# Kernel tuning notes

Hardware: AMD Instinct MI355X
Metric: run time of the kernel (lower is better)

Reference implementation:

```python
import jax, jax.numpy as jnp
import numpy as np
import math

EPS = 1e-6          # eps for safe cumprod / clamping
CHUNK = 4           # chunk_size w
SHARP = 1.0         # sharpening_factor
NOISE_STD = 1.0
N_HEADS = 4
ADIM = 512


def moving_sum(x, back, forward):
    """Windowed running sum over last axis: out[k] = sum_{j=k-back}^{k+forward} x[j].
    Equivalent to the conv1d trick in the original (all-ones filter)."""
    k = x.shape[-1]
    pad = [(0, 0)] * (x.ndim - 1) + [(back, forward)]
    c = jnp.cumsum(jnp.pad(x, pad), axis=-1)
    c0 = jnp.concatenate([jnp.zeros_like(c[..., :1]), c], axis=-1)
    w = back + forward
    return c0[..., w + 1: w + 1 + k] - c0[..., :k]


def setup_inputs() -> dict:
    rng = jax.random.key(0)
    ks = jax.random.split(rng, 12)
    B, qlen, klen, kdim, qdim, adim = 8, 256, 2048, 512, 512, ADIM
    s = 0.02
    return {
        "key_enc": jax.random.normal(ks[0], (B, klen, kdim), jnp.float32),
        "query":   jax.random.normal(ks[1], (B, qlen, qdim), jnp.float32),
        "noise":   jax.random.normal(ks[2], (B, qlen, klen), jnp.float32),
        # monotonic energy params
        "Wk_m": jax.random.normal(ks[3], (kdim, adim), jnp.float32) * s,
        "bk_m": jnp.zeros((adim,), jnp.float32),
        "Wq_m": jax.random.normal(ks[4], (qdim, adim), jnp.float32) * s,
        "bq_m": jnp.zeros((adim,), jnp.float32),
        "r":    jnp.array([-4.0], jnp.float32),
        # chunkwise energy params (multi-head)
        "Wk_c": jax.random.normal(ks[5], (kdim, adim), jnp.float32) * s,
        "bk_c": jnp.zeros((adim,), jnp.float32),
        "Wq_c": jax.random.normal(ks[6], (qdim, adim), jnp.float32) * s,
        "bq_c": jnp.zeros((adim,), jnp.float32),
    }


def _mocha_beta(key_enc, query, noise, Wk_m, bk_m, Wq_m, bq_m, r,
                Wk_c, bk_c, Wq_c, bq_c):
    B, klen, _ = key_enc.shape
    qlen = query.shape[1]
    H = N_HEADS
    dk = ADIM // H
    scale = math.sqrt(ADIM)

    # --- monotonic energy (single head): [B, qlen, klen]
    k_m = key_enc @ Wk_m + bk_m
    q_m = query @ Wq_m + bq_m
    e_mono = jnp.einsum('bqa,bka->bqk', q_m, k_m) / scale + r[0]

    # --- p_choose with additive gaussian noise (encourages discreteness)
    p_choose = jax.nn.sigmoid(e_mono + noise * NOISE_STD)  # [B,q,k]

    # --- safe cumprod of (1 - p) via exclusive cumsum in log space
    log1mp = jnp.log(jnp.clip(1.0 - p_choose, EPS, 1.0))
    cumprod_1mp = jnp.exp(jnp.cumsum(log1mp, axis=-1) - log1mp)  # exclusive

    # --- monotonic alpha recurrence over query steps (parallel-mode MoChA)
    aw0 = jnp.zeros((B, klen), jnp.float32).at[:, 0].set(1.0)

    def step(aw_prev, inp):
        p_i, cp_i = inp  # [B, klen]
        alpha_i = p_i * cp_i * jnp.cumsum(
            aw_prev / jnp.clip(cp_i, EPS, 1.0), axis=-1)
        return alpha_i, alpha_i

    xs = (jnp.swapaxes(p_choose, 0, 1), jnp.swapaxes(cumprod_1mp, 0, 1))
    _, alpha_q = jax.lax.scan(step, aw0, xs)          # [q, B, k]
    alpha = jnp.swapaxes(alpha_q, 0, 1)                # [B, q, k]

    # --- chunkwise energy (multi-head): [B, H, q, k]
    k_c = (key_enc @ Wk_c + bk_c).reshape(B, klen, H, dk)
    q_c = (query @ Wq_c + bq_c).reshape(B, qlen, H, dk)
    e_chunk = jnp.einsum('bqhd,bkhd->bhqk', q_c, k_c) / scale

    # --- efficient chunkwise attention (clipped-logit moving-sum softmax)
    e = e_chunk - jnp.max(e_chunk, axis=3, keepdims=True)
    softmax_exp = jnp.maximum(jnp.exp(e), 1e-5)
    denom = moving_sum(softmax_exp, back=CHUNK - 1, forward=0)
    beta = softmax_exp * moving_sum(
        alpha[:, None] * SHARP / denom, back=0, forward=CHUNK - 1)
    return beta  # [B, H, q, k]


def reference(key_enc, query, noise, Wk_m, bk_m, Wq_m, bq_m, r,
              Wk_c, bk_c, Wq_c, bq_c):
    return _mocha_beta(key_enc, query, noise, Wk_m, bk_m, Wq_m, bq_m, r,
                       Wk_c, bk_c, Wq_c, bq_c)
```

## Files before the change

### kernel.cpp

```cpp
#include <hip/hip_runtime.h>
#include <math.h>

#define BATCH   8
#define QLEN    256
#define KLEN    2048
#define KDIM    512
#define ADIMC   512
#define NHEADS  4
#define DKH     128
#define CHUNKW  4

static constexpr float INV_SCALE = 0.04419417382415922f;
static constexpr float EPSV = 1e-6f;

typedef __attribute__((ext_vector_type(8))) short bf16x8;
typedef __attribute__((ext_vector_type(4))) float f32x4;

__device__ __forceinline__ unsigned short f2bf(float f) {
    unsigned u = __builtin_bit_cast(unsigned, f);
    u += 0x7fffu + ((u >> 16) & 1u);
    return (unsigned short)(u >> 16);
}

__device__ __forceinline__ void lds_barrier() {
    __asm__ volatile("s_waitcnt lgkmcnt(0)\n\ts_barrier" ::: "memory");
}

__device__ __forceinline__ void gload_lds16(const void* g, void* l) {
    __builtin_amdgcn_global_load_lds(
        (const __attribute__((address_space(1))) void*)g,
        (__attribute__((address_space(3))) void*)l, 16, 0, 0);
}

__global__ __launch_bounds__(256) void cast_bf16(
    const float* __restrict__ x, unsigned short* __restrict__ y, int n4)
{
    int i = blockIdx.x * 256 + threadIdx.x;
    if (i < n4) {
        float4 v = ((const float4*)x)[i];
        ushort4 o;
        o.x = f2bf(v.x); o.y = f2bf(v.y); o.z = f2bf(v.z); o.w = f2bf(v.w);
        ((ushort4*)y)[i] = o;
    }
}

__global__ __launch_bounds__(256) void transpose_cast(
    const float* __restrict__ W, unsigned short* __restrict__ WT)
{
    __shared__ float tile[32][33];
    const int tx = threadIdx.x;
    const int ty = threadIdx.y;
    const int k0 = blockIdx.y * 32, n0 = blockIdx.x * 32;
    #pragma unroll
    for (int i = 0; i < 32; i += 8)
        tile[ty + i][tx] = W[(size_t)(k0 + ty + i) * KDIM + n0 + tx];
    __syncthreads();
    #pragma unroll
    for (int i = 0; i < 32; i += 8)
        WT[(size_t)(n0 + ty + i) * KDIM + k0 + tx] = f2bf(tile[tx][ty + i]);
}

template<int KSTEPS>
__device__ __forceinline__ void mfma_nt_staged(
    const unsigned short* __restrict__ A, const unsigned short* __restrict__ B,
    int lda, int ldb, int bm, int bn,
    unsigned short* AsLDS, unsigned short* BsLDS, f32x4 acc[4][4])
{
    const int t = threadIdx.x;
    const int wv = t >> 6, ln = t & 63;
    const int r = ln & 15, quad = ln >> 4;
    const int wm = (wv >> 1) * 64, wn = (wv & 1) * 64;
    const int srow = wv * 16 + (ln >> 2);
    const int scol = (ln & 3) * 8;

    for (int ks = 0; ks < KSTEPS; ++ks) {
        const int k0 = ks * 32;
        #pragma unroll
        for (int j = 0; j < 2; ++j) {
            gload_lds16(A + (size_t)(bm + j * 64 + srow) * lda + k0 + scol,
                        AsLDS + (size_t)(j * 64 + wv * 16) * 32);
            gload_lds16(B + (size_t)(bn + j * 64 + srow) * ldb + k0 + scol,
                        BsLDS + (size_t)(j * 64 + wv * 16) * 32);
        }
        __syncthreads();
        bf16x8 af[4], bg[4];
        #pragma unroll
        for (int f = 0; f < 4; ++f)
            af[f] = *(const bf16x8*)(AsLDS + (size_t)(wm + f * 16 + r) * 32 + quad * 8);
        #pragma unroll
        for (int f = 0; f < 4; ++f)
            bg[f] = *(const bf16x8*)(BsLDS + (size_t)(wn + f * 16 + r) * 32 + quad * 8);
        #pragma unroll
        for (int i = 0; i < 4; ++i)
            #pragma unroll
            for (int j2 = 0; j2 < 4; ++j2)
                acc[i][j2] = __builtin_amdgcn_mfma_f32_16x16x32_bf16(
                    af[i], bg[j2], acc[i][j2], 0, 0, 0);
        __syncthreads();
    }
}

__device__ __forceinline__ void zero_acc(f32x4 acc[4][4]) {
    #pragma unroll
    for (int i = 0; i < 4; ++i)
        #pragma unroll
        for (int j = 0; j < 4; ++j)
            acc[i][j] = f32x4{0.f, 0.f, 0.f, 0.f};
}

__global__ __launch_bounds__(256) void proj_mfma(
    const unsigned short* __restrict__ A, const unsigned short* __restrict__ WT,
    const float* __restrict__ bias_m, const float* __restrict__ bias_c,
    unsigned short* __restrict__ C)
{
    __shared__ unsigned short As[128 * 32];
    __shared__ unsigned short Bs[128 * 32];
    const int bm = blockIdx.y * 128, bn = blockIdx.x * 128;
    f32x4 acc[4][4]; zero_acc(acc);
    mfma_nt_staged<16>(A, WT, KDIM, KDIM, bm, bn, As, Bs, acc);
    const int wv = threadIdx.x >> 6, ln = threadIdx.x & 63;
    const int r = ln & 15, quad = ln >> 4;
    const int m0 = bm + (wv >> 1) * 64, n0 = bn + (wv & 1) * 64;
    #pragma unroll
    for (int j = 0; j < 4; ++j) {
        const int n = n0 + j * 16 + r;
        const float bv = (n < 512) ? bias_m[n] : bias_c[n - 512];
        #pragma unroll
        for (int i = 0; i < 4; ++i) {
            #pragma unroll
            for (int reg = 0; reg < 4; ++reg) {
                const int m = m0 + i * 16 + quad * 4 + reg;
                C[(size_t)m * 1024 + n] = f2bf(acc[i][j][reg] + bv);
            }
        }
    }
}

__global__ __launch_bounds__(256) void pchoose_mfma(
    const unsigned short* __restrict__ qp, const unsigned short* __restrict__ kp,
    const float* __restrict__ noise, const float* __restrict__ rp,
    float* __restrict__ p)
{
    __shared__ unsigned short As[128 * 32];
    __shared__ unsigned short Bs[128 * 32];
    const int b = blockIdx.z;
    const unsigned short* A = qp + (size_t)b * QLEN * 1024;
    const unsigned short* B = kp + (size_t)b * KLEN * 1024;
    const int bm = blockIdx.y * 128, bn = blockIdx.x * 128;
    f32x4 acc[4][4]; zero_acc(acc);
    mfma_nt_staged<16>(A, B, 1024, 1024, bm, bn, As, Bs, acc);
    const int wv = threadIdx.x >> 6, ln = threadIdx.x & 63;
    const int r = ln & 15, quad = ln >> 4;
    const int m0 = bm + (wv >> 1) * 64, n0 = bn + (wv & 1) * 64;
    const float rv = rp[0];
    #pragma unroll
    for (int i = 0; i < 4; ++i) {
        #pragma unroll
        for (int reg = 0; reg < 4; ++reg) {
            const int q = m0 + i * 16 + quad * 4 + reg;
            const size_t rowoff = ((size_t)b * QLEN + q) * KLEN;
            #pragma unroll
            for (int j = 0; j < 4; ++j) {
                const int k = n0 + j * 16 + r;
                const float e = acc[i][j][reg] * INV_SCALE + rv + noise[rowoff + k];
                p[rowoff + k] = __builtin_amdgcn_rcpf(1.0f + __expf(-e));
            }
        }
    }
}

__device__ __forceinline__ float wave_incl_scan(float x)
{
#define DPP_ADD(ctrl, rmask, bctrl)                                            \
    { int _t = __builtin_amdgcn_update_dpp(0, __builtin_bit_cast(int, x),      \
                                           ctrl, rmask, 0xf, bctrl);           \
      x += __builtin_bit_cast(float, _t); }
    DPP_ADD(0x111, 0xf, true)
    DPP_ADD(0x112, 0xf, true)
    DPP_ADD(0x114, 0xf, true)
    DPP_ADD(0x118, 0xf, true)
    DPP_ADD(0x142, 0xa, false)
    DPP_ADD(0x143, 0xc, false)
#undef DPP_ADD
    return x;
}

__global__ __launch_bounds__(256) void cumprod_mr(
    const float* __restrict__ p, float* __restrict__ mArr, float* __restrict__ rArr)
{
    const size_t row = blockIdx.x;
    const float* pr = p + row * KLEN;
    float* mr = mArr + row * KLEN;
    float* rr = rArr + row * KLEN;
    const int tid = threadIdx.x;
    const int lane = tid & 63, wid = tid >> 6;
    __shared__ float waveTot[4];

    float4 v0 = *(const float4*)(pr + tid * 8);
    float4 v1 = *(const float4*)(pr + tid * 8 + 4);
    float pv[8] = {v0.x, v0.y, v0.z, v0.w, v1.x, v1.y, v1.z, v1.w};
    float excl[8];
    float run = 0.0f;
    #pragma unroll
    for (int j = 0; j < 8; ++j) {
        float l = __logf(fminf(fmaxf(1.0f - pv[j], EPSV), 1.0f));
        excl[j] = run;
        run += l;
    }
    float s = wave_incl_scan(run);
    if (lane == 63) waveTot[wid] = s;
    __syncthreads();
    float wex = 0.0f;
    for (int w = 0; w < wid; ++w) wex += waveTot[w];
    const float texcl = wex + s - run;

    float mv[8], rv[8];
    #pragma unroll
    for (int j = 0; j < 8; ++j) {
        const float cpv = __expf(texcl + excl[j]);
        mv[j] = pv[j] * cpv;
        rv[j] = __builtin_amdgcn_rcpf(fminf(fmaxf(cpv, EPSV), 1.0f));
    }
    *(float4*)(mr + tid * 8)     = *(float4*)&mv[0];
    *(float4*)(mr + tid * 8 + 4) = *(float4*)&mv[4];
    *(float4*)(rr + tid * 8)     = *(float4*)&rv[0];
    *(float4*)(rr + tid * 8 + 4) = *(float4*)&rv[4];
}

__global__ __launch_bounds__(512, 1) void alpha_echunk(
    const float* __restrict__ mArr, const float* __restrict__ rArr,
    float* __restrict__ alpha,
    const unsigned short* __restrict__ qp, const unsigned short* __restrict__ kp,
    float* __restrict__ out)
{
    __shared__ __align__(16) char smem[98304];
    const int bid = blockIdx.x;
    const int tid = threadIdx.x;

    if (bid < BATCH) {
        __builtin_amdgcn_s_setprio(1);
        float (*wt)[8] = (float (*)[8])smem;
        const int lane = tid & 63, wid = tid >> 6;
        const float* mrow = mArr + (size_t)bid * QLEN * KLEN + tid * 4;
        const float* rrow = rArr + (size_t)bid * QLEN * KLEN + tid * 4;
        float* arow = alpha + (size_t)bid * QLEN * KLEN + tid * 4;

        float aw0 = 0.f, aw1 = 0.f, aw2 = 0.f, aw3 = 0.f;
        if (tid == 0) aw0 = 1.0f;

        float4 mA = *(const float4*)(mrow);
        float4 rA = *(const float4*)(rrow);
        float4 mB = *(const float4*)(mrow + KLEN);
        float4 rB = *(const float4*)(rrow + KLEN);

#define ASTEP(I, MREG, RREG)                                                   \
    {                                                                          \
        const int i_ = (I);                                                    \
        float4 mc = MREG, rc = RREG;                                           \
        const int rn_ = (i_ + 2 < QLEN) ? (i_ + 2) : (QLEN - 1);               \
        MREG = *(const float4*)(mrow + (size_t)rn_ * KLEN);                    \
        RREG = *(const float4*)(rrow + (size_t)rn_ * KLEN);                    \
        float run = 0.0f, i0, i1, i2, i3;                                      \
        run = fmaf(aw0, rc.x, run); i0 = run;                                  \
        run = fmaf(aw1, rc.y, run); i1 = run;                                  \
        run = fmaf(aw2, rc.z, run); i2 = run;                                  \
        run = fmaf(aw3, rc.w, run); i3 = run;                                  \
        float tot = wave_incl_scan(run);                                       \
        if (lane == 63) wt[i_ & 1][wid] = tot;                                 \
        lds_barrier();                                                         \
        float base = tot - run;                                                \
        float4 w0 = *(const float4*)&wt[i_ & 1][0];                            \
        float4 w1 = *(const float4*)&wt[i_ & 1][4];                            \
        if (wid > 0) base += w0.x;                                             \
        if (wid > 1) base += w0.y;                                             \
        if (wid > 2) base += w0.z;                                             \
        if (wid > 3) base += w0.w;                                             \
        if (wid > 4) base += w1.x;                                             \
        if (wid > 5) base += w1.y;                                             \
        if (wid > 6) base += w1.z;                                             \
        aw0 = mc.x * (base + i0);                                              \
        aw1 = mc.y * (base + i1);                                              \
        aw2 = mc.z * (base + i2);                                              \
        aw3 = mc.w * (base + i3);                                              \
        float4 ov; ov.x = aw0; ov.y = aw1; ov.z = aw2; ov.w = aw3;             \
        *(float4*)(arow + (size_t)i_ * KLEN) = ov;                             \
    }

        for (int io = 0; io < QLEN; io += 2) {
            ASTEP(io + 0, mA, rA)
            ASTEP(io + 1, mB, rB)
        }
#undef ASTEP
        __builtin_amdgcn_s_setprio(0);
        return;
    }

    const int v = bid - BATCH;
    const int z = v >> 5;
    const int by = (v >> 4) & 1;
    const int bx = v & 15;
    const int b = z >> 2, h = z & 3;
    const bool worker = tid < 256;
    unsigned short* As = (unsigned short*)smem;
    unsigned short* Bs = (unsigned short*)(smem + 8192);
    const unsigned short* A = qp + (size_t)b * QLEN * 1024 + 512 + h * DKH;
    const unsigned short* B = kp + (size_t)b * KLEN * 1024 + 512 + h * DKH;
    const int bm = by * 128, bn = bx * 128;

    const int wv = tid >> 6, ln = tid & 63;
    const int r = ln & 15, quad = ln >> 4;
    const int wm = (wv >> 1) * 64, wn = (wv & 1) * 64;
    const int srow = (wv & 3) * 16 + (ln >> 2);
    const int scol = (ln & 3) * 8;

    f32x4 acc[4][4]; zero_acc(acc);
    for (int ks = 0; ks < 4; ++ks) {
        const int k0 = ks * 32;
        if (worker) {
            #pragma unroll
            for (int j = 0; j < 2; ++j) {
                gload_lds16(A + (size_t)(bm + j * 64 + srow) * 1024 + k0 + scol,
                            As + (size_t)(j * 64 + wv * 16) * 32);
                gload_lds16(B + (size_t)(bn + j * 64 + srow) * 1024 + k0 + scol,
                            Bs + (size_t)(j * 64 + wv * 16) * 32);
            }
        }
        __syncthreads();
        if (worker) {
            bf16x8 af[4], bg[4];
            #pragma unroll
            for (int f = 0; f < 4; ++f)
                af[f] = *(const bf16x8*)(As + (size_t)(wm + f * 16 + r) * 32 + quad * 8);
            #pragma unroll
            for (int f = 0; f < 4; ++f)
                bg[f] = *(const bf16x8*)(Bs + (size_t)(wn + f * 16 + r) * 32 + quad * 8);
            #pragma unroll
            for (int i = 0; i < 4; ++i)
                #pragma unroll
                for (int j2 = 0; j2 < 4; ++j2)
                    acc[i][j2] = __builtin_amdgcn_mfma_f32_16x16x32_bf16(
                        af[i], bg[j2], acc[i][j2], 0, 0, 0);
        }
        __syncthreads();
    }
    if (worker) {
        const int m0 = bm + (wv >> 1) * 64, n0 = bn + (wv & 1) * 64;
        #pragma unroll
        for (int i = 0; i < 4; ++i) {
            #pragma unroll
            for (int reg = 0; reg < 4; ++reg) {
                const int q = m0 + i * 16 + quad * 4 + reg;
                const size_t rowoff = ((size_t)z * QLEN + q) * KLEN;
                #pragma unroll
                for (int j = 0; j < 4; ++j) {
                    const int k = n0 + j * 16 + r;
                    out[rowoff + k] = acc[i][j][reg] * INV_SCALE;
                }
            }
        }
    }
}

__global__ __launch_bounds__(256) void beta_kernel(
    float* __restrict__ eo, const float* __restrict__ alpha)
{
    __shared__ float sse[KLEN + 3];
    __shared__ float su[KLEN + 3];
    __shared__ float wmax[4];

    const int tid = threadIdx.x;
    const int lane = tid & 63, wid = tid >> 6;
    const int row = blockIdx.x;
    const int q = row & (QLEN - 1);
    const int b = row >> 10;
    float* erow = eo + (size_t)row * KLEN;
    const float* arow = alpha + ((size_t)b * QLEN + q) * KLEN;

    if (tid < 3) { sse[tid] = 0.0f; su[KLEN + tid] = 0.0f; }

// ... 21 lines not shown
    #pragma unroll
    for (int j = 0; j < 8; ++j) {
        const int k = tid + 256 * j;
        const float denom = sse[k + 3] + sse[k + 2] + sse[k + 1] + sse[k];
        su[k] = arow[k] * __builtin_amdgcn_rcpf(denom);
    }
    __syncthreads();

    #pragma unroll
    for (int j = 0; j < 8; ++j) {
        const int k = tid + 256 * j;
        erow[k] = sse[k + 3] * (su[k] + su[k + 1] + su[k + 2] + su[k + 3]);
    }
}

extern "C" void kernel_launch(void* const* d_in, const int* in_sizes, int n_in,
                              void* d_out, int out_size, void* d_ws, size_t ws_size,
                              hipStream_t stream)
{
    (void)in_sizes; (void)n_in; (void)out_size; (void)ws_size;
    const float* key_enc = (const float*)d_in[0];
    const float* query   = (const float*)d_in[1];
    const float* noise   = (const float*)d_in[2];
    const float* Wk_m    = (const float*)d_in[3];
    const float* bk_m    = (const float*)d_in[4];
    const float* Wq_m    = (const float*)d_in[5];
    const float* bq_m    = (const float*)d_in[6];
    const float* rp      = (const float*)d_in[7];
    const float* Wk_c    = (const float*)d_in[8];
    const float* bk_c    = (const float*)d_in[9];
    const float* Wq_c    = (const float*)d_in[10];
    const float* bq_c    = (const float*)d_in[11];
    float* out = (float*)d_out;

    char* w = (char*)d_ws;
    unsigned short* kx    = (unsigned short*)w; w += (size_t)BATCH * KLEN * KDIM * 2;
    unsigned short* qx    = (unsigned short*)w; w += (size_t)BATCH * QLEN * KDIM * 2;
    unsigned short* WTk   = (unsigned short*)w; w += (size_t)1024 * KDIM * 2;
    unsigned short* WTq   = (unsigned short*)w; w += (size_t)1024 * KDIM * 2;
    unsigned short* kproj = (unsigned short*)w; w += (size_t)BATCH * KLEN * 1024 * 2;
    unsigned short* qproj = (unsigned short*)w; w += (size_t)BATCH * QLEN * 1024 * 2;
    float* p_alpha = (float*)w; w += (size_t)BATCH * QLEN * KLEN * 4;
    float* mArr    = (float*)w; w += (size_t)BATCH * QLEN * KLEN * 4;
    float* rArr    = (float*)w;

    hipLaunchKernelGGL(cast_bf16, dim3(BATCH * KLEN * KDIM / 4 / 256), dim3(256), 0, stream,
                       key_enc, kx, BATCH * KLEN * KDIM / 4);
    hipLaunchKernelGGL(cast_bf16, dim3(BATCH * QLEN * KDIM / 4 / 256), dim3(256), 0, stream,
                       query, qx, BATCH * QLEN * KDIM / 4);
    hipLaunchKernelGGL(transpose_cast, dim3(16, 16), dim3(32, 8), 0, stream, Wk_m, WTk);
    hipLaunchKernelGGL(transpose_cast, dim3(16, 16), dim3(32, 8), 0, stream, Wk_c, WTk + (size_t)512 * KDIM);
    hipLaunchKernelGGL(transpose_cast, dim3(16, 16), dim3(32, 8), 0, stream, Wq_m, WTq);
    hipLaunchKernelGGL(transpose_cast, dim3(16, 16), dim3(32, 8), 0, stream, Wq_c, WTq + (size_t)512 * KDIM);

    hipLaunchKernelGGL(proj_mfma, dim3(8, BATCH * KLEN / 128), dim3(256), 0, stream,
                       kx, WTk, bk_m, bk_c, kproj);
    hipLaunchKernelGGL(proj_mfma, dim3(8, BATCH * QLEN / 128), dim3(256), 0, stream,
                       qx, WTq, bq_m, bq_c, qproj);

    hipLaunchKernelGGL(pchoose_mfma, dim3(KLEN / 128, QLEN / 128, BATCH), dim3(256), 0, stream,
                       qproj, kproj, noise, rp, p_alpha);

    hipLaunchKernelGGL(cumprod_mr, dim3(BATCH * QLEN), dim3(256), 0, stream,
                       p_alpha, mArr, rArr);

    hipLaunchKernelGGL(alpha_echunk, dim3(BATCH + KLEN / 128 * QLEN / 128 * BATCH * NHEADS),
                       dim3(512), 0, stream,
                       mArr, rArr, p_alpha, qproj, kproj, out);

    hipLaunchKernelGGL(beta_kernel, dim3(BATCH * NHEADS * QLEN), dim3(256), 0, stream,
                       out, p_alpha);
}
```

Before: 307.6 us.

## Replace per-step block barrier in alpha scan with LDS flag-chained wave prefix passing

The sequential alpha recurrence used a block-wide s_barrier each query step to combine the eight waves' partial sums. It now uses a decoupled chained scan: each wave spins on a 64-bit LDS slot holding the previous wave's inclusive prefix tagged with the step index, then publishes its own. This removes the full-block barrier from the critical path but makes the waves a serial chain and adds volatile LDS polling. It also costs one up-front zeroing pass over QLEN*8 slots.

```diff
diff --git a/kernel.cpp b/kernel.cpp
--- a/kernel.cpp
+++ b/kernel.cpp
@@ -20,10 +20,6 @@
     unsigned u = __builtin_bit_cast(unsigned, f);
     u += 0x7fffu + ((u >> 16) & 1u);
     return (unsigned short)(u >> 16);
-}
-
-__device__ __forceinline__ void lds_barrier() {
-    __asm__ volatile("s_waitcnt lgkmcnt(0)\n\ts_barrier" ::: "memory");
 }
 
 __device__ __forceinline__ void gload_lds16(const void* g, void* l) {
@@ -238,13 +234,19 @@
     const int tid = threadIdx.x;
 
     if (bid < BATCH) {
+        unsigned long long* slots = (unsigned long long*)smem;
+        for (int idx = tid; idx < QLEN * 8; idx += 512) slots[idx] = 0ULL;
+        __syncthreads();
+
         __builtin_amdgcn_s_setprio(1);
-        float (*wt)[8] = (float (*)[8])smem;
         const int lane = tid & 63, wid = tid >> 6;
         const float* mrow = mArr + (size_t)bid * QLEN * KLEN + tid * 4;
         const float* rrow = rArr + (size_t)bid * QLEN * KLEN + tid * 4;
         float* arow = alpha + (size_t)bid * QLEN * KLEN + tid * 4;
 
+        volatile unsigned long long* psl  = slots + ((wid > 0) ? (wid - 1) : 0);
+        volatile unsigned long long* pslw = slots + wid;
+
         float aw0 = 0.f, aw1 = 0.f, aw2 = 0.f, aw3 = 0.f;
         if (tid == 0) aw0 = 1.0f;
 
@@ -256,6 +258,8 @@
 #define ASTEP(I, MREG, RREG)                                                   \
     {                                                                          \
         const int i_ = (I);                                                    \
+        unsigned long long v_ = 0ULL;                                          \
+        if (wid > 0) v_ = *psl;             \
         float4 mc = MREG, rc = RREG;                                           \
         const int rn_ = (i_ + 2 < QLEN) ? (i_ + 2) : (QLEN - 1);               \
         MREG = *(const float4*)(mrow + (size_t)rn_ * KLEN);                    \
@@ -265,23 +269,21 @@
         run = fmaf(aw1, rc.y, run); i1 = run;                                  \
         run = fmaf(aw2, rc.z, run); i2 = run;                                  \
         run = fmaf(aw3, rc.w, run); i3 = run;                                  \
-        float tot = wave_incl_scan(run);                                       \
-        if (lane == 63) wt[i_ & 1][wid] = tot;                                 \
-        lds_barrier();                                                         \
-        float base = tot - run;                                                \
-        float4 w0 = *(const float4*)&wt[i_ & 1][0];                            \
-        float4 w1 = *(const float4*)&wt[i_ & 1][4];                            \
-        if (wid > 0) base += w0.x;                                             \
-        if (wid > 1) base += w0.y;                                             \
-        if (wid > 2) base += w0.z;                                             \
-        if (wid > 3) base += w0.w;                                             \
-        if (wid > 4) base += w1.x;                                             \
-        if (wid > 5) base += w1.y;                                             \
-        if (wid > 6) base += w1.z;                                             \
-        aw0 = mc.x * (base + i0);                                              \
-        aw1 = mc.y * (base + i1);                                              \
-        aw2 = mc.z * (base + i2);                                              \
-        aw3 = mc.w * (base + i3);                                              \
+        float s_ = wave_incl_scan(run);                                        \
+        float base = 0.0f;                                                     \
+        if (wid > 0) {                                                         \
+            while ((unsigned)(v_ >> 32) != (unsigned)(i_ + 1)) v_ = *psl;      \
+            base = __builtin_bit_cast(float, (unsigned)v_);                    \
+        }                                                                      \
+        if (wid < 7 && lane == 63)                                             \
+            *pslw = ((unsigned long long)(unsigned)(i_ + 1) << 32)             \
+                  | (unsigned long long)__builtin_bit_cast(unsigned, base + s_);\
+        psl += 8; pslw += 8;                                                   \
+        const float wb = base + (s_ - run);                                    \
+        aw0 = mc.x * (wb + i0);                                                \
+        aw1 = mc.y * (wb + i1);                                                \
+        aw2 = mc.z * (wb + i2);                                                \
+        aw3 = mc.w * (wb + i3);                                                \
         float4 ov; ov.x = aw0; ov.y = aw1; ov.z = aw2; ov.w = aw3;             \
         *(float4*)(arow + (size_t)i_ * KLEN) = ov;                             \
     }
```

After: 402.2 us. 30.8% more time.

## Merge prep and projection launches; shrink alpha_echunk blocks to 256 threads

Applied to the files above, without the earlier changes.

The two cast kernels and four transpose-cast kernels become one prep launch, and the two projection GEMMs become one launch split by block row, cutting launch count and letting small grids share the device. The alpha_echunk kernel goes from 512 to 256 threads: the serial alpha scan now handles 8 columns per thread over 4 waves, which shortens the cross-wave reduction. The e_chunk GEMM blocks lose their idle half of threads. The risk is a longer per-thread serial chain in the scan, which sits on the critical path.

```diff
diff --git a/kernel.cpp b/kernel.cpp
--- a/kernel.cpp
+++ b/kernel.cpp
@@ -32,25 +32,40 @@
         (__attribute__((address_space(3))) void*)l, 16, 0, 0);
 }
 
-__global__ __launch_bounds__(256) void cast_bf16(
-    const float* __restrict__ x, unsigned short* __restrict__ y, int n4)
-{
-    int i = blockIdx.x * 256 + threadIdx.x;
-    if (i < n4) {
+#define NKXB (BATCH * KLEN * KDIM / 4 / 256)
+#define NQXB (BATCH * QLEN * KDIM / 4 / 256)
+__global__ __launch_bounds__(256) void prep(
+    const float* __restrict__ key_enc, const float* __restrict__ query,
+    const float* __restrict__ Wk_m, const float* __restrict__ Wk_c,
+    const float* __restrict__ Wq_m, const float* __restrict__ Wq_c,
+    unsigned short* __restrict__ kx, unsigned short* __restrict__ qx,
+    unsigned short* __restrict__ WTk, unsigned short* __restrict__ WTq)
+{
+    __shared__ float tile[32][33];
+    const int gb = blockIdx.x;
+    const int tid = threadIdx.x;
+
+    if (gb < NKXB + NQXB) {
+        const float* x = (gb < NKXB) ? key_enc : query;
+        unsigned short* y = (gb < NKXB) ? kx : qx;
+        const int i = (gb < NKXB ? gb : gb - NKXB) * 256 + tid;
         float4 v = ((const float4*)x)[i];
         ushort4 o;
         o.x = f2bf(v.x); o.y = f2bf(v.y); o.z = f2bf(v.z); o.w = f2bf(v.w);
         ((ushort4*)y)[i] = o;
-    }
-}
-
-__global__ __launch_bounds__(256) void transpose_cast(
-    const float* __restrict__ W, unsigned short* __restrict__ WT)
-{
-    __shared__ float tile[32][33];
-    const int tx = threadIdx.x;
-    const int ty = threadIdx.y;
-    const int k0 = blockIdx.y * 32, n0 = blockIdx.x * 32;
+        return;
+    }
+    const int t = gb - NKXB - NQXB;
+    const int which = t >> 8;
+    const int tt = t & 255;
+    const int bx = tt & 15, byy = tt >> 4;
+    const float* W = (which == 0) ? Wk_m : (which == 1) ? Wk_c
+                   : (which == 2) ? Wq_m : Wq_c;
+    unsigned short* WT = (which == 0) ? WTk
+                       : (which == 1) ? WTk + (size_t)512 * KDIM
+                       : (which == 2) ? WTq : WTq + (size_t)512 * KDIM;
+    const int tx = tid & 31, ty = tid >> 5;
+    const int k0 = byy * 32, n0 = bx * 32;
     #pragma unroll
     for (int i = 0; i < 32; i += 8)
         tile[ty + i][tx] = W[(size_t)(k0 + ty + i) * KDIM + n0 + tx];
@@ -109,13 +124,22 @@
 }
 
 __global__ __launch_bounds__(256) void proj_mfma(
-    const unsigned short* __restrict__ A, const unsigned short* __restrict__ WT,
-    const float* __restrict__ bias_m, const float* __restrict__ bias_c,
-    unsigned short* __restrict__ C)
+    const unsigned short* __restrict__ kx, const unsigned short* __restrict__ qx,
+    const unsigned short* __restrict__ WTk, const unsigned short* __restrict__ WTq,
+    const float* __restrict__ bk_m, const float* __restrict__ bk_c,
+    const float* __restrict__ bq_m, const float* __restrict__ bq_c,
+    unsigned short* __restrict__ kproj, unsigned short* __restrict__ qproj)
 {
     __shared__ unsigned short As[128 * 32];
     __shared__ unsigned short Bs[128 * 32];
-    const int bm = blockIdx.y * 128, bn = blockIdx.x * 128;
+    const int by = blockIdx.y;
+    const unsigned short *A, *WT;
+    unsigned short* C;
+    const float *bm_, *bc_;
+    int bm;
+    if (by < 128) { A = kx; WT = WTk; C = kproj; bm_ = bk_m; bc_ = bk_c; bm = by * 128; }
+    else          { A = qx; WT = WTq; C = qproj; bm_ = bq_m; bc_ = bq_c; bm = (by - 128) * 128; }
+    const int bn = blockIdx.x * 128;
     f32x4 acc[4][4]; zero_acc(acc);
     mfma_nt_staged<16>(A, WT, KDIM, KDIM, bm, bn, As, Bs, acc);
     const int wv = threadIdx.x >> 6, ln = threadIdx.x & 63;
@@ -124,7 +148,7 @@
     #pragma unroll
     for (int j = 0; j < 4; ++j) {
         const int n = n0 + j * 16 + r;
-        const float bv = (n < 512) ? bias_m[n] : bias_c[n - 512];
+        const float bv = (n < 512) ? bm_[n] : bc_[n - 512];
         #pragma unroll
         for (int i = 0; i < 4; ++i) {
             #pragma unroll
@@ -227,7 +251,7 @@
     *(float4*)(rr + tid * 8 + 4) = *(float4*)&rv[4];
 }
 
-__global__ __launch_bounds__(512, 1) void alpha_echunk(
+__global__ __launch_bounds__(256, 1) void alpha_echunk(
     const float* __restrict__ mArr, const float* __restrict__ rArr,
     float* __restrict__ alpha,
     const unsigned short* __restrict__ qp, const unsigned short* __restrict__ kp,
@@ -239,56 +263,68 @@
 
     if (bid < BATCH) {
         __builtin_amdgcn_s_setprio(1);
-        float (*wt)[8] = (float (*)[8])smem;
+        float (*wt)[4] = (float (*)[4])smem;
         const int lane = tid & 63, wid = tid >> 6;
-        const float* mrow = mArr + (size_t)bid * QLEN * KLEN + tid * 4;
-        const float* rrow = rArr + (size_t)bid * QLEN * KLEN + tid * 4;
-        float* arow = alpha + (size_t)bid * QLEN * KLEN + tid * 4;
+        const float* mrow = mArr + (size_t)bid * QLEN * KLEN + tid * 8;
+        const float* rrow = rArr + (size_t)bid * QLEN * KLEN + tid * 8;
+        float* arow = alpha + (size_t)bid * QLEN * KLEN + tid * 8;
 
         float aw0 = 0.f, aw1 = 0.f, aw2 = 0.f, aw3 = 0.f;
+        float aw4 = 0.f, aw5 = 0.f, aw6 = 0.f, aw7 = 0.f;
         if (tid == 0) aw0 = 1.0f;
 
-        float4 mA = *(const float4*)(mrow);
-        float4 rA = *(const float4*)(rrow);
-        float4 mB = *(const float4*)(mrow + KLEN);
-        float4 rB = *(const float4*)(rrow + KLEN);
-
-#define ASTEP(I, MREG, RREG)                                                   \
+        float4 mA0 = *(const float4*)(mrow);
+        float4 mA1 = *(const float4*)(mrow + 4);
+        float4 rA0 = *(const float4*)(rrow);
+        float4 rA1 = *(const float4*)(rrow + 4);
+        float4 mB0 = *(const float4*)(mrow + KLEN);
+        float4 mB1 = *(const float4*)(mrow + KLEN + 4);
+        float4 rB0 = *(const float4*)(rrow + KLEN);
+        float4 rB1 = *(const float4*)(rrow + KLEN + 4);
+
+#define ASTEP(I, M0, M1, R0, R1)                                               \
     {                                                                          \
         const int i_ = (I);                                                    \
-        float4 mc = MREG, rc = RREG;                                           \
+        float4 mc0 = M0, mc1 = M1, rc0 = R0, rc1 = R1;                         \
         const int rn_ = (i_ + 2 < QLEN) ? (i_ + 2) : (QLEN - 1);               \
-        MREG = *(const float4*)(mrow + (size_t)rn_ * KLEN);                    \
-        RREG = *(const float4*)(rrow + (size_t)rn_ * KLEN);                    \
-        float run = 0.0f, i0, i1, i2, i3;                                      \
-        run = fmaf(aw0, rc.x, run); i0 = run;                                  \
-        run = fmaf(aw1, rc.y, run); i1 = run;                                  \
-        run = fmaf(aw2, rc.z, run); i2 = run;                                  \
-        run = fmaf(aw3, rc.w, run); i3 = run;                                  \
+        M0 = *(const float4*)(mrow + (size_t)rn_ * KLEN);                      \
+        M1 = *(const float4*)(mrow + (size_t)rn_ * KLEN + 4);                  \
+        R0 = *(const float4*)(rrow + (size_t)rn_ * KLEN);                      \
+        R1 = *(const float4*)(rrow + (size_t)rn_ * KLEN + 4);                  \
+        float run = 0.0f, i0, i1, i2, i3, i4, i5, i6, i7;                      \
+        run = fmaf(aw0, rc0.x, run); i0 = run;                                 \
+        run = fmaf(aw1, rc0.y, run); i1 = run;                                 \
+        run = fmaf(aw2, rc0.z, run); i2 = run;                                 \
+        run = fmaf(aw3, rc0.w, run); i3 = run;                                 \
+        run = fmaf(aw4, rc1.x, run); i4 = run;                                 \
+        run = fmaf(aw5, rc1.y, run); i5 = run;                                 \
+        run = fmaf(aw6, rc1.z, run); i6 = run;                                 \
+        run = fmaf(aw7, rc1.w, run); i7 = run;                                 \
         float tot = wave_incl_scan(run);                                       \
         if (lane == 63) wt[i_ & 1][wid] = tot;                                 \
         lds_barrier();                                                         \
         float base = tot - run;                                                \
         float4 w0 = *(const float4*)&wt[i_ & 1][0];                            \
-        float4 w1 = *(const float4*)&wt[i_ & 1][4];                            \
         if (wid > 0) base += w0.x;                                             \
         if (wid > 1) base += w0.y;                                             \
         if (wid > 2) base += w0.z;                                             \
-        if (wid > 3) base += w0.w;                                             \
-        if (wid > 4) base += w1.x;                                             \
-        if (wid > 5) base += w1.y;                                             \
-        if (wid > 6) base += w1.z;                                             \
-        aw0 = mc.x * (base + i0);                                              \
-        aw1 = mc.y * (base + i1);                                              \
-        aw2 = mc.z * (base + i2);                                              \
-        aw3 = mc.w * (base + i3);                                              \
-        float4 ov; ov.x = aw0; ov.y = aw1; ov.z = aw2; ov.w = aw3;             \
-        *(float4*)(arow + (size_t)i_ * KLEN) = ov;                             \
+        aw0 = mc0.x * (base + i0);                                             \
+        aw1 = mc0.y * (base + i1);                                             \
+        aw2 = mc0.z * (base + i2);                                             \
+        aw3 = mc0.w * (base + i3);                                             \
+        aw4 = mc1.x * (base + i4);                                             \
+        aw5 = mc1.y * (base + i5);                                             \
+        aw6 = mc1.z * (base + i6);                                             \
+        aw7 = mc1.w * (base + i7);                                             \
+        float4 ov0; ov0.x = aw0; ov0.y = aw1; ov0.z = aw2; ov0.w = aw3;        \
+        float4 ov1; ov1.x = aw4; ov1.y = aw5; ov1.z = aw6; ov1.w = aw7;        \
+        *(float4*)(arow + (size_t)i_ * KLEN)     = ov0;                        \
+        *(float4*)(arow + (size_t)i_ * KLEN + 4) = ov1;                        \
     }
 
         for (int io = 0; io < QLEN; io += 2) {
-            ASTEP(io + 0, mA, rA)
-            ASTEP(io + 1, mB, rB)
+            ASTEP(io + 0, mA0, mA1, rA0, rA1)
+            ASTEP(io + 1, mB0, mB1, rB0, rB1)
         }
 #undef ASTEP
         __builtin_amdgcn_s_setprio(0);
@@ -300,7 +336,6 @@
     const int by = (v >> 4) & 1;
     const int bx = v & 15;
     const int b = z >> 2, h = z & 3;
-    const bool worker = tid < 256;
     unsigned short* As = (unsigned short*)smem;
     unsigned short* Bs = (unsigned short*)(smem + 8192);
     const unsigned short* A = qp + (size_t)b * QLEN * 1024 + 512 + h * DKH;
@@ -310,40 +345,36 @@
     const int wv = tid >> 6, ln = tid & 63;
     const int r = ln & 15, quad = ln >> 4;
     const int wm = (wv >> 1) * 64, wn = (wv & 1) * 64;
-    const int srow = (wv & 3) * 16 + (ln >> 2);
+    const int srow = wv * 16 + (ln >> 2);
     const int scol = (ln & 3) * 8;
 
     f32x4 acc[4][4]; zero_acc(acc);
     for (int ks = 0; ks < 4; ++ks) {
         const int k0 = ks * 32;
-        if (worker) {
+        #pragma unroll
+        for (int j = 0; j < 2; ++j) {
+            gload_lds16(A + (size_t)(bm + j * 64 + srow) * 1024 + k0 + scol,
+                        As + (size_t)(j * 64 + wv * 16) * 32);
+            gload_lds16(B + (size_t)(bn + j * 64 + srow) * 1024 + k0 + scol,
+                        Bs + (size_t)(j * 64 + wv * 16) * 32);
+        }
+        __syncthreads();
+        bf16x8 af[4], bg[4];
+        #pragma unroll
+        for (int f = 0; f < 4; ++f)
+            af[f] = *(const bf16x8*)(As + (size_t)(wm + f * 16 + r) * 32 + quad * 8);
+        #pragma unroll
+        for (int f = 0; f < 4; ++f)
+            bg[f] = *(const bf16x8*)(Bs + (size_t)(wn + f * 16 + r) * 32 + quad * 8);
+        #pragma unroll
+        for (int i = 0; i < 4; ++i)
             #pragma unroll
-            for (int j = 0; j < 2; ++j) {
-                gload_lds16(A + (size_t)(bm + j * 64 + srow) * 1024 + k0 + scol,
-                            As + (size_t)(j * 64 + wv * 16) * 32);
-                gload_lds16(B + (size_t)(bn + j * 64 + srow) * 1024 + k0 + scol,
-                            Bs + (size_t)(j * 64 + wv * 16) * 32);
-            }
-        }
+            for (int j2 = 0; j2 < 4; ++j2)
+                acc[i][j2] = __builtin_amdgcn_mfma_f32_16x16x32_bf16(
+                    af[i], bg[j2], acc[i][j2], 0, 0, 0);
         __syncthreads();
-        if (worker) {
-            bf16x8 af[4], bg[4];
-            #pragma unroll
-            for (int f = 0; f < 4; ++f)
-                af[f] = *(const bf16x8*)(As + (size_t)(wm + f * 16 + r) * 32 + quad * 8);
-            #pragma unroll
-            for (int f = 0; f < 4; ++f)
-                bg[f] = *(const bf16x8*)(Bs + (size_t)(wn + f * 16 + r) * 32 + quad * 8);
-            #pragma unroll
-            for (int i = 0; i < 4; ++i)
-                #pragma unroll
-                for (int j2 = 0; j2 < 4; ++j2)
-                    acc[i][j2] = __builtin_amdgcn_mfma_f32_16x16x32_bf16(
-                        af[i], bg[j2], acc[i][j2], 0, 0, 0);
-        }
-        __syncthreads();
-    }
-    if (worker) {
+    }
+    {
         const int m0 = bm + (wv >> 1) * 64, n0 = bn + (wv & 1) * 64;
         #pragma unroll
         for (int i = 0; i < 4; ++i) {
@@ -444,19 +475,13 @@
     float* mArr    = (float*)w; w += (size_t)BATCH * QLEN * KLEN * 4;
     float* rArr    = (float*)w;
 
-    hipLaunchKernelGGL(cast_bf16, dim3(BATCH * KLEN * KDIM / 4 / 256), dim3(256), 0, stream,
-                       key_enc, kx, BATCH * KLEN * KDIM / 4);
-    hipLaunchKernelGGL(cast_bf16, dim3(BATCH * QLEN * KDIM / 4 / 256), dim3(256), 0, stream,
-                       query, qx, BATCH * QLEN * KDIM / 4);
-    hipLaunchKernelGGL(transpose_cast, dim3(16, 16), dim3(32, 8), 0, stream, Wk_m, WTk);
-    hipLaunchKernelGGL(transpose_cast, dim3(16, 16), dim3(32, 8), 0, stream, Wk_c, WTk + (size_t)512 * KDIM);
-    hipLaunchKernelGGL(transpose_cast, dim3(16, 16), dim3(32, 8), 0, stream, Wq_m, WTq);
-    hipLaunchKernelGGL(transpose_cast, dim3(16, 16), dim3(32, 8), 0, stream, Wq_c, WTq + (size_t)512 * KDIM);
-
-    hipLaunchKernelGGL(proj_mfma, dim3(8, BATCH * KLEN / 128), dim3(256), 0, stream,
-                       kx, WTk, bk_m, bk_c, kproj);
-    hipLaunchKernelGGL(proj_mfma, dim3(8, BATCH * QLEN / 128), dim3(256), 0, stream,
-                       qx, WTq, bq_m, bq_c, qproj);
+    hipLaunchKernelGGL(prep, dim3(NKXB + NQXB + 1024), dim3(256), 0, stream,
+                       key_enc, query, Wk_m, Wk_c, Wq_m, Wq_c,
+                       kx, qx, WTk, WTq);
+
+    hipLaunchKernelGGL(proj_mfma, dim3(8, BATCH * KLEN / 128 + BATCH * QLEN / 128),
+                       dim3(256), 0, stream,
+                       kx, qx, WTk, WTq, bk_m, bk_c, bq_m, bq_c, kproj, qproj);
 
     hipLaunchKernelGGL(pchoose_mfma, dim3(KLEN / 128, QLEN / 128, BATCH), dim3(256), 0, stream,
                        qproj, kproj, noise, rp, p_alpha);
@@ -465,7 +490,7 @@
                        p_alpha, mArr, rArr);
 
     hipLaunchKernelGGL(alpha_echunk, dim3(BATCH + KLEN / 128 * QLEN / 128 * BATCH * NHEADS),
-                       dim3(512), 0, stream,
+                       dim3(256), 0, stream,
                        mArr, rArr, p_alpha, qproj, kproj, out);
 
     hipLaunchKernelGGL(beta_kernel, dim3(BATCH * NHEADS * QLEN), dim3(256), 0, stream,
```

After: 296.6 us. 3.6% less time.

## Reassociate projections: fold key weights into query side, skip key projection GEMM

Applied to the files above, without the earlier changes.

Rather than projecting the large key tensor (B*2048 rows) through both weight matrices, precompute G = Wq·Wk^T per segment and per head, so that q·G can be multiplied directly against the raw bf16 keys. Bias cross-terms are folded into a per-column offset, and a per-query scalar replaces the bias terms in the monotonic energy. This removes the 16K-row key projection GEMM and its bf16 writeback, plus the weight transposes, in exchange for a wider query-side matrix (5×512 columns) and a K=512 inner loop in the chunk energy GEMM instead of 128. The cast kernels are merged into one launch, and the chunk-energy tiles become 128x256 using all 8 waves.

```diff
diff --git a/kernel.cpp b/kernel.cpp
--- a/kernel.cpp
+++ b/kernel.cpp
@@ -5,10 +5,11 @@
 #define QLEN    256
 #define KLEN    2048
 #define KDIM    512
-#define ADIMC   512
 #define NHEADS  4
 #define DKH     128
-#define CHUNKW  4
+#define NG      5
+#define QROWS   (BATCH * QLEN)
+#define GCOLS   (NG * 512)
 
 static constexpr float INV_SCALE = 0.04419417382415922f;
 static constexpr float EPSV = 1e-6f;
@@ -21,6 +22,10 @@
     u += 0x7fffu + ((u >> 16) & 1u);
     return (unsigned short)(u >> 16);
 }
+__device__ __forceinline__ float bf2f(unsigned short u) {
+    unsigned x = (unsigned)u << 16;
+    return __builtin_bit_cast(float, x);
+}
 
 __device__ __forceinline__ void lds_barrier() {
     __asm__ volatile("s_waitcnt lgkmcnt(0)\n\ts_barrier" ::: "memory");
@@ -32,39 +37,37 @@
         (__attribute__((address_space(3))) void*)l, 16, 0, 0);
 }
 
-__global__ __launch_bounds__(256) void cast_bf16(
-    const float* __restrict__ x, unsigned short* __restrict__ y, int n4)
-{
-    int i = blockIdx.x * 256 + threadIdx.x;
-    if (i < n4) {
-        float4 v = ((const float4*)x)[i];
-        ushort4 o;
-        o.x = f2bf(v.x); o.y = f2bf(v.y); o.z = f2bf(v.z); o.w = f2bf(v.w);
-        ((ushort4*)y)[i] = o;
-    }
-}
-
-__global__ __launch_bounds__(256) void transpose_cast(
-    const float* __restrict__ W, unsigned short* __restrict__ WT)
-{
-    __shared__ float tile[32][33];
-    const int tx = threadIdx.x;
-    const int ty = threadIdx.y;
-    const int k0 = blockIdx.y * 32, n0 = blockIdx.x * 32;
-    #pragma unroll
-    for (int i = 0; i < 32; i += 8)
-        tile[ty + i][tx] = W[(size_t)(k0 + ty + i) * KDIM + n0 + tx];
-    __syncthreads();
-    #pragma unroll
-    for (int i = 0; i < 32; i += 8)
-        WT[(size_t)(n0 + ty + i) * KDIM + k0 + tx] = f2bf(tile[tx][ty + i]);
-}
-
-template<int KSTEPS>
+#define NKXB 8192
+#define NQXB 1024
+__global__ __launch_bounds__(256) void prep(
+    const float* __restrict__ key_enc, const float* __restrict__ query,
+    const float* __restrict__ Wk_m, const float* __restrict__ Wk_c,
+    const float* __restrict__ Wq_m, const float* __restrict__ Wq_c,
+    unsigned short* __restrict__ kx, unsigned short* __restrict__ qx,
+    unsigned short* __restrict__ kwm, unsigned short* __restrict__ kwc,
+    unsigned short* __restrict__ qwm, unsigned short* __restrict__ qwc)
+{
+    const int gb = blockIdx.x, tid = threadIdx.x;
+    const float* x; unsigned short* y; int i;
+    if (gb < NKXB)              { x = key_enc; y = kx; i = gb * 256 + tid; }
+    else if (gb < NKXB + NQXB)  { x = query;   y = qx; i = (gb - NKXB) * 256 + tid; }
+    else {
+        const int w = gb - NKXB - NQXB;
+        const int which = w >> 8;
+        i = (w & 255) * 256 + tid;
+        x = (which == 0) ? Wk_m : (which == 1) ? Wk_c : (which == 2) ? Wq_m : Wq_c;
+        y = (which == 0) ? kwm  : (which == 1) ? kwc  : (which == 2) ? qwm  : qwc;
+    }
+    float4 v = ((const float4*)x)[i];
+    ushort4 o;
+    o.x = f2bf(v.x); o.y = f2bf(v.y); o.z = f2bf(v.z); o.w = f2bf(v.w);
+    ((ushort4*)y)[i] = o;
+}
+
 __device__ __forceinline__ void mfma_nt_staged(
     const unsigned short* __restrict__ A, const unsigned short* __restrict__ B,
     int lda, int ldb, int bm, int bn,
-    unsigned short* AsLDS, unsigned short* BsLDS, f32x4 acc[4][4])
+    unsigned short* AsLDS, unsigned short* BsLDS, f32x4 acc[4][4], int ksteps)
 {
     const int t = threadIdx.x;
     const int wv = t >> 6, ln = t & 63;
@@ -73,7 +76,7 @@
     const int srow = wv * 16 + (ln >> 2);
     const int scol = (ln & 3) * 8;
 
-    for (int ks = 0; ks < KSTEPS; ++ks) {
+    for (int ks = 0; ks < ksteps; ++ks) {
         const int k0 = ks * 32;
         #pragma unroll
         for (int j = 0; j < 2; ++j) {
@@ -108,47 +111,150 @@
             acc[i][j] = f32x4{0.f, 0.f, 0.f, 0.f};
 }
 
-__global__ __launch_bounds__(256) void proj_mfma(
-    const unsigned short* __restrict__ A, const unsigned short* __restrict__ WT,
-    const float* __restrict__ bias_m, const float* __restrict__ bias_c,
-    unsigned short* __restrict__ C)
+__global__ __launch_bounds__(256) void smallg(
+    const unsigned short* __restrict__ kwm, const unsigned short* __restrict__ kwc,
+    const unsigned short* __restrict__ qwm, const unsigned short* __restrict__ qwc,
+    const float* __restrict__ Wk_mf, const float* __restrict__ Wk_cf,
+    const float* __restrict__ Wq_mf,
+    const float* __restrict__ bq_m, const float* __restrict__ bk_m,
+    const float* __restrict__ bq_c,
+    unsigned short* __restrict__ GT, float* __restrict__ aux)
 {
     __shared__ unsigned short As[128 * 32];
     __shared__ unsigned short Bs[128 * 32];
-    const int bm = blockIdx.y * 128, bn = blockIdx.x * 128;
-    f32x4 acc[4][4]; zero_acc(acc);
-    mfma_nt_staged<16>(A, WT, KDIM, KDIM, bm, bn, As, Bs, acc);
-    const int wv = threadIdx.x >> 6, ln = threadIdx.x & 63;
-    const int r = ln & 15, quad = ln >> 4;
-    const int m0 = bm + (wv >> 1) * 64, n0 = bn + (wv & 1) * 64;
-    #pragma unroll
-    for (int j = 0; j < 4; ++j) {
-        const int n = n0 + j * 16 + r;
-        const float bv = (n < 512) ? bias_m[n] : bias_c[n - 512];
-        #pragma unroll
-        for (int i = 0; i < 4; ++i) {
+    __shared__ float red[256];
+    const int blk = blockIdx.x, tid = threadIdx.x;
+
+    if (blk < 80) {
+        const int seg = blk >> 4, t = blk & 15;
+        const int bm = (t >> 2) * 128, bn = (t & 3) * 128;
+        const unsigned short *A, *B; int ks;
+        if (seg == 0) { A = kwm; B = qwm; ks = 16; }
+        else { const int h = seg - 1; A = kwc + h * 128; B = qwc + h * 128; ks = 4; }
+        f32x4 acc[4][4]; zero_acc(acc);
+        mfma_nt_staged(A, B, 512, 512, bm, bn, As, Bs, acc, ks);
+        const int wv = tid >> 6, ln = tid & 63;
+        const int r = ln & 15, quad = ln >> 4;
+        const int m0 = bm + (wv >> 1) * 64, n0 = bn + (wv & 1) * 64;
+        #pragma unroll
+        for (int j = 0; j < 4; ++j) {
+            const int n = n0 + j * 16 + r;
             #pragma unroll
-            for (int reg = 0; reg < 4; ++reg) {
-                const int m = m0 + i * 16 + quad * 4 + reg;
-                C[(size_t)m * 1024 + n] = f2bf(acc[i][j][reg] + bv);
-            }
-        }
-    }
+            for (int i = 0; i < 4; ++i)
+                #pragma unroll
+                for (int reg = 0; reg < 4; ++reg) {
+                    const int m = m0 + i * 16 + quad * 4 + reg;
+                    GT[(size_t)(seg * 512 + m) * 512 + n] = f2bf(acc[i][j][reg]);
+                }
+        }
+        return;
+    }
+    const int ab = blk - 80;
+    if (ab < 2) {
+        const int d = ab * 256 + tid;
+        const float* row = Wk_mf + (size_t)d * 512;
+        float s = 0.f;
+        for (int j = 0; j < 512; j += 4) {
+            float4 a = *(const float4*)(row + j);
+            float4 b = *(const float4*)(bq_m + j);
+            s += a.x * b.x + a.y * b.y + a.z * b.z + a.w * b.w;
+        }
+        aux[d] = s; return;
+    }
+    if (ab < 10) {
+        const int t = ab - 2, h = t >> 1;
+        const int d = (t & 1) * 256 + tid;
+        const float* row = Wk_cf + (size_t)d * 512 + h * 128;
+        const float* bv = bq_c + h * 128;
+        float s = 0.f;
+        for (int j = 0; j < 128; j += 4) {
+            float4 a = *(const float4*)(row + j);
+            float4 b = *(const float4*)(bv + j);
+            s += a.x * b.x + a.y * b.y + a.z * b.z + a.w * b.w;
+        }
+        aux[512 + h * 512 + d] = s; return;
+    }
+    if (ab < 12) {
+        const int d = (ab - 10) * 256 + tid;
+        const float* row = Wq_mf + (size_t)d * 512;
+        float s = 0.f;
+        for (int j = 0; j < 512; j += 4) {
+            float4 a = *(const float4*)(row + j);
+            float4 b = *(const float4*)(bk_m + j);
+            s += a.x * b.x + a.y * b.y + a.z * b.z + a.w * b.w;
+        }
+        aux[GCOLS + d] = s; return;
+    }
+    float s = bq_m[tid] * bk_m[tid] + bq_m[tid + 256] * bk_m[tid + 256];
+    red[tid] = s; __syncthreads();
+    for (int o = 128; o > 0; o >>= 1) {
+        if (tid < o) red[tid] += red[tid + o];
+        __syncthreads();
+    }
+    if (tid == 0) aux[GCOLS + 512] = red[0];
+}
+
+__global__ __launch_bounds__(256) void qg_kernel(
+    const unsigned short* __restrict__ qx, const unsigned short* __restrict__ GT,
+    const float* __restrict__ aux,
+    unsigned short* __restrict__ qg, float* __restrict__ vq2)
+{
+    __shared__ unsigned short As[128 * 32];
+    __shared__ unsigned short Bs[128 * 32];
+    __shared__ float wuS[512];
+    const int v = blockIdx.x, tid = threadIdx.x;
+    if (v < 320) {
+        const int by = v / 20, bx = v % 20;
+        const int bm = by * 128, bn = bx * 128;
+        f32x4 acc[4][4]; zero_acc(acc);
+        mfma_nt_staged(qx, GT, 512, 512, bm, bn, As, Bs, acc, 16);
+        const int wv = tid >> 6, ln = tid & 63;
+        const int r = ln & 15, quad = ln >> 4;
+        const int m0 = bm + (wv >> 1) * 64, n0 = bn + (wv & 1) * 64;
+        #pragma unroll
+        for (int j = 0; j < 4; ++j) {
+            const int n = n0 + j * 16 + r;
+            const float wvb = aux[n];
+            #pragma unroll
+            for (int i = 0; i < 4; ++i)
+                #pragma unroll
+                for (int reg = 0; reg < 4; ++reg) {
+                    const int m = m0 + i * 16 + quad * 4 + reg;
+                    qg[(size_t)m * GCOLS + n] = f2bf(acc[i][j][reg] + wvb);
+                }
+        }
+        return;
+    }
+    wuS[tid] = aux[GCOLS + tid];
+    wuS[tid + 256] = aux[GCOLS + tid + 256];
+    __syncthreads();
+    const float cc = aux[GCOLS + 512];
+    const int q = (v - 320) * 256 + tid;
+    const unsigned short* row = qx + (size_t)q * 512;
+    float s = 0.f;
+    for (int j = 0; j < 512; j += 4) {
+        ushort4 a = *(const ushort4*)(row + j);
+        s = fmaf(bf2f(a.x), wuS[j], s);
+        s = fmaf(bf2f(a.y), wuS[j + 1], s);
+        s = fmaf(bf2f(a.z), wuS[j + 2], s);
+        s = fmaf(bf2f(a.w), wuS[j + 3], s);
+    }
+    vq2[q] = (s + cc) * INV_SCALE;
 }
 
 __global__ __launch_bounds__(256) void pchoose_mfma(
-    const unsigned short* __restrict__ qp, const unsigned short* __restrict__ kp,
+    const unsigned short* __restrict__ qg, const unsigned short* __restrict__ kx,
     const float* __restrict__ noise, const float* __restrict__ rp,
-    float* __restrict__ p)
+    const float* __restrict__ vq2, float* __restrict__ p)
 {
     __shared__ unsigned short As[128 * 32];
     __shared__ unsigned short Bs[128 * 32];
     const int b = blockIdx.z;
-    const unsigned short* A = qp + (size_t)b * QLEN * 1024;
-    const unsigned short* B = kp + (size_t)b * KLEN * 1024;
+    const unsigned short* A = qg + (size_t)b * QLEN * GCOLS;
+    const unsigned short* B = kx + (size_t)b * KLEN * 512;
     const int bm = blockIdx.y * 128, bn = blockIdx.x * 128;
     f32x4 acc[4][4]; zero_acc(acc);
-    mfma_nt_staged<16>(A, B, 1024, 1024, bm, bn, As, Bs, acc);
+    mfma_nt_staged(A, B, GCOLS, 512, bm, bn, As, Bs, acc, 16);
     const int wv = threadIdx.x >> 6, ln = threadIdx.x & 63;
     const int r = ln & 15, quad = ln >> 4;
     const int m0 = bm + (wv >> 1) * 64, n0 = bn + (wv & 1) * 64;
@@ -159,10 +265,11 @@
         for (int reg = 0; reg < 4; ++reg) {
             const int q = m0 + i * 16 + quad * 4 + reg;
             const size_t rowoff = ((size_t)b * QLEN + q) * KLEN;
+            const float vq = vq2[b * QLEN + q] + rv;
             #pragma unroll
             for (int j = 0; j < 4; ++j) {
                 const int k = n0 + j * 16 + r;
-                const float e = acc[i][j][reg] * INV_SCALE + rv + noise[rowoff + k];
+                const float e = acc[i][j][reg] * INV_SCALE + vq + noise[rowoff + k];
                 p[rowoff + k] = __builtin_amdgcn_rcpf(1.0f + __expf(-e));
             }
         }
@@ -230,7 +337,7 @@
 __global__ __launch_bounds__(512, 1) void alpha_echunk(
     const float* __restrict__ mArr, const float* __restrict__ rArr,
     float* __restrict__ alpha,
-    const unsigned short* __restrict__ qp, const unsigned short* __restrict__ kp,
+    const unsigned short* __restrict__ qg, const unsigned short* __restrict__ kx,
     float* __restrict__ out)
 {
     __shared__ __align__(16) char smem[98304];
@@ -296,55 +403,50 @@
     }
 
     const int v = bid - BATCH;
-    const int z = v >> 5;
-    const int by = (v >> 4) & 1;
-    const int bx = v & 15;
+    const int z = v >> 4;
+    const int rest = v & 15;
+    const int by = rest >> 3;
+    const int bx = rest & 7;
     const int b = z >> 2, h = z & 3;
-    const bool worker = tid < 256;
     unsigned short* As = (unsigned short*)smem;
     unsigned short* Bs = (unsigned short*)(smem + 8192);
-    const unsigned short* A = qp + (size_t)b * QLEN * 1024 + 512 + h * DKH;
-    const unsigned short* B = kp + (size_t)b * KLEN * 1024 + 512 + h * DKH;
-    const int bm = by * 128, bn = bx * 128;
-
-    const int wv = tid >> 6, ln = tid & 63;
+    const unsigned short* A = qg + (size_t)(b * QLEN) * GCOLS + 512 + h * 512;
+    const unsigned short* B = kx + (size_t)b * KLEN * 512;
+    const int bm = by * 128, bn = bx * 256;
+
+    const int wv8 = tid >> 6, ln = tid & 63;
     const int r = ln & 15, quad = ln >> 4;
-    const int wm = (wv >> 1) * 64, wn = (wv & 1) * 64;
-    const int srow = (wv & 3) * 16 + (ln >> 2);
+    const int wr = wv8 >> 2, wc = wv8 & 3;
+    const int srow = tid >> 2;
     const int scol = (ln & 3) * 8;
 
     f32x4 acc[4][4]; zero_acc(acc);
-    for (int ks = 0; ks < 4; ++ks) {
+    for (int ks = 0; ks < 16; ++ks) {
         const int k0 = ks * 32;
-        if (worker) {
+        gload_lds16(A + (size_t)(bm + srow) * GCOLS + k0 + scol,
+                    As + (size_t)wv8 * 512);
+        gload_lds16(B + (size_t)(bn + srow) * 512 + k0 + scol,
+                    Bs + (size_t)wv8 * 512);
+        gload_lds16(B + (size_t)(bn + 128 + srow) * 512 + k0 + scol,
+                    Bs + 4096 + (size_t)wv8 * 512);
+        __syncthreads();
+        bf16x8 af[4], bg[4];
+        #pragma unroll
+        for (int f = 0; f < 4; ++f)
+            af[f] = *(const bf16x8*)(As + (size_t)(wr * 64 + f * 16 + r) * 32 + quad * 8);
+        #pragma unroll
+        for (int f = 0; f < 4; ++f)
+            bg[f] = *(const bf16x8*)(Bs + (size_t)(wc * 64 + f * 16 + r) * 32 + quad * 8);
+        #pragma unroll
+        for (int i = 0; i < 4; ++i)
             #pragma unroll
-            for (int j = 0; j < 2; ++j) {
-                gload_lds16(A + (size_t)(bm + j * 64 + srow) * 1024 + k0 + scol,
-                            As + (size_t)(j * 64 + wv * 16) * 32);
-                gload_lds16(B + (size_t)(bn + j * 64 + srow) * 1024 + k0 + scol,
-                            Bs + (size_t)(j * 64 + wv * 16) * 32);
-            }
-        }
+            for (int j2 = 0; j2 < 4; ++j2)
+                acc[i][j2] = __builtin_amdgcn_mfma_f32_16x16x32_bf16(
+                    af[i], bg[j2], acc[i][j2], 0, 0, 0);
         __syncthreads();
-        if (worker) {
-            bf16x8 af[4], bg[4];
-            #pragma unroll
-            for (int f = 0; f < 4; ++f)
-                af[f] = *(const bf16x8*)(As + (size_t)(wm + f * 16 + r) * 32 + quad * 8);
-            #pragma unroll
-            for (int f = 0; f < 4; ++f)
-                bg[f] = *(const bf16x8*)(Bs + (size_t)(wn + f * 16 + r) * 32 + quad * 8);
-            #pragma unroll
-            for (int i = 0; i < 4; ++i)
-                #pragma unroll
-                for (int j2 = 0; j2 < 4; ++j2)
-                    acc[i][j2] = __builtin_amdgcn_mfma_f32_16x16x32_bf16(
-                        af[i], bg[j2], acc[i][j2], 0, 0, 0);
-        }
-        __syncthreads();
-    }
-    if (worker) {
-        const int m0 = bm + (wv >> 1) * 64, n0 = bn + (wv & 1) * 64;
+    }
+    {
+        const int m0 = bm + wr * 64, n0 = bn + wc * 64;
         #pragma unroll
         for (int i = 0; i < 4; ++i) {
             #pragma unroll
@@ -432,41 +534,42 @@
     const float* Wq_c    = (const float*)d_in[10];
     const float* bq_c    = (const float*)d_in[11];
     float* out = (float*)d_out;
+    (void)bk_c;
 
     char* w = (char*)d_ws;
-    unsigned short* kx    = (unsigned short*)w; w += (size_t)BATCH * KLEN * KDIM * 2;
-    unsigned short* qx    = (unsigned short*)w; w += (size_t)BATCH * QLEN * KDIM * 2;
-    unsigned short* WTk   = (unsigned short*)w; w += (size_t)1024 * KDIM * 2;
-    unsigned short* WTq   = (unsigned short*)w; w += (size_t)1024 * KDIM * 2;
-    unsigned short* kproj = (unsigned short*)w; w += (size_t)BATCH * KLEN * 1024 * 2;
-    unsigned short* qproj = (unsigned short*)w; w += (size_t)BATCH * QLEN * 1024 * 2;
+    unsigned short* kx   = (unsigned short*)w; w += (size_t)BATCH * KLEN * KDIM * 2;
+    unsigned short* qx   = (unsigned short*)w; w += (size_t)QROWS * KDIM * 2;
+    unsigned short* kwm  = (unsigned short*)w; w += (size_t)512 * 512 * 2;
+    unsigned short* kwc  = (unsigned short*)w; w += (size_t)512 * 512 * 2;
+    unsigned short* qwm  = (unsigned short*)w; w += (size_t)512 * 512 * 2;
+    unsigned short* qwc  = (unsigned short*)w; w += (size_t)512 * 512 * 2;
+    unsigned short* GT   = (unsigned short*)w; w += (size_t)GCOLS * 512 * 2;
+    unsigned short* qg   = (unsigned short*)w; w += (size_t)QROWS * GCOLS * 2;
+    float* aux    = (float*)w; w += 4096 * 4;
+    float* vq2    = (float*)w; w += QROWS * 4;
     float* p_alpha = (float*)w; w += (size_t)BATCH * QLEN * KLEN * 4;
     float* mArr    = (float*)w; w += (size_t)BATCH * QLEN * KLEN * 4;
     float* rArr    = (float*)w;
 
-    hipLaunchKernelGGL(cast_bf16, dim3(BATCH * KLEN * KDIM / 4 / 256), dim3(256), 0, stream,
-                       key_enc, kx, BATCH * KLEN * KDIM / 4);
-    hipLaunchKernelGGL(cast_bf16, dim3(BATCH * QLEN * KDIM / 4 / 256), dim3(256), 0, stream,
-                       query, qx, BATCH * QLEN * KDIM / 4);
-    hipLaunchKernelGGL(transpose_cast, dim3(16, 16), dim3(32, 8), 0, stream, Wk_m, WTk);
-    hipLaunchKernelGGL(transpose_cast, dim3(16, 16), dim3(32, 8), 0, stream, Wk_c, WTk + (size_t)512 * KDIM);
-    hipLaunchKernelGGL(transpose_cast, dim3(16, 16), dim3(32, 8), 0, stream, Wq_m, WTq);
-    hipLaunchKernelGGL(transpose_cast, dim3(16, 16), dim3(32, 8), 0, stream, Wq_c, WTq + (size_t)512 * KDIM);
-
-    hipLaunchKernelGGL(proj_mfma, dim3(8, BATCH * KLEN / 128), dim3(256), 0, stream,
-                       kx, WTk, bk_m, bk_c, kproj);
-    hipLaunchKernelGGL(proj_mfma, dim3(8, BATCH * QLEN / 128), dim3(256), 0, stream,
-                       qx, WTq, bq_m, bq_c, qproj);
+    hipLaunchKernelGGL(prep, dim3(NKXB + NQXB + 1024), dim3(256), 0, stream,
+                       key_enc, query, Wk_m, Wk_c, Wq_m, Wq_c,
+                       kx, qx, kwm, kwc, qwm, qwc);
+
+    hipLaunchKernelGGL(smallg, dim3(93), dim3(256), 0, stream,
+                       kwm, kwc, qwm, qwc, Wk_m, Wk_c, Wq_m,
+                       bq_m, bk_m, bq_c, GT, aux);
+
+    hipLaunchKernelGGL(qg_kernel, dim3(328), dim3(256), 0, stream,
+                       qx, GT, aux, qg, vq2);
 
     hipLaunchKernelGGL(pchoose_mfma, dim3(KLEN / 128, QLEN / 128, BATCH), dim3(256), 0, stream,
-                       qproj, kproj, noise, rp, p_alpha);
+                       qg, kx, noise, rp, vq2, p_alpha);
 
     hipLaunchKernelGGL(cumprod_mr, dim3(BATCH * QLEN), dim3(256), 0, stream,
                        p_alpha, mArr, rArr);
 
-    hipLaunchKernelGGL(alpha_echunk, dim3(BATCH + KLEN / 128 * QLEN / 128 * BATCH * NHEADS),
-                       dim3(512), 0, stream,
-                       mArr, rArr, p_alpha, qproj, kproj, out);
+    hipLaunchKernelGGL(alpha_echunk, dim3(BATCH + 512), dim3(512), 0, stream,
+                       mArr, rArr, p_alpha, qg, kx, out);
 
     hipLaunchKernelGGL(beta_kernel, dim3(BATCH * NHEADS * QLEN), dim3(256), 0, stream,
                        out, p_alpha);
```

Measured after the change: 282.9 us. 1.09x faster.
